# Performance work log

Hardware: AMD Instinct MI355X
Metric: run time of the kernel (lower is better)

Reference implementation:

```python
import jax, jax.numpy as jnp
import numpy as np

NUM_NOD = 6
MAX_PREV = 5
NUM_EDGE = 20  # (1+5)*5//2 + 5*(6-5)
D = 1024
H = 8
LN_EPS = 1e-6


def setup_inputs() -> dict:
    key = jax.random.key(0)
    ks = jax.random.split(key, 12)
    B, S = 8, 1024
    scale = 1.0 / np.sqrt(D)
    return {
        "inputs": jax.random.normal(ks[0], (B, S, D), jnp.float32),
        "ew": jax.random.uniform(ks[1], (NUM_NOD, 3), jnp.float32),
        "act_w": jax.random.uniform(ks[2], (NUM_NOD,), jnp.float32),
        "We": jax.random.normal(ks[3], (NUM_EDGE, D, D), jnp.float32) * scale,
        "be": jnp.zeros((NUM_EDGE, D), jnp.float32),
        "Wq": jax.random.normal(ks[4], (NUM_NOD, D, D), jnp.float32) * scale,
        "Wk": jax.random.normal(ks[5], (NUM_NOD, D, D), jnp.float32) * scale,
        "Wv": jax.random.normal(ks[6], (NUM_NOD, D, D), jnp.float32) * scale,
        "Wo": jax.random.normal(ks[7], (NUM_NOD, D, D), jnp.float32) * scale,
        "ln_g": jnp.ones((D,), jnp.float32),
        "ln_b": jnp.zeros((D,), jnp.float32),
    }


def _layernorm(x, g, b):
    mu = jnp.mean(x, axis=-1, keepdims=True)
    var = jnp.mean(jnp.square(x - mu), axis=-1, keepdims=True)
    return (x - mu) * jax.lax.rsqrt(var + LN_EPS) * g + b


def _mha(q, k, v, wq, wk, wv, wo):
    B, S, d = q.shape
    dh = d // H
    qh = (q @ wq).reshape(B, S, H, dh)
    kh = (k @ wk).reshape(B, S, H, dh)
    vh = (v @ wv).reshape(B, S, H, dh)
    scores = jnp.einsum("bqhd,bkhd->bhqk", qh, kh) / jnp.sqrt(jnp.asarray(dh, q.dtype))
    attn = jax.nn.softmax(scores, axis=-1)
    ctx = jnp.einsum("bhqk,bkhd->bqhd", attn, vh).reshape(B, S, d)
    return ctx @ wo


def reference(inputs, ew, act_w, We, be, Wq, Wk, Wv, Wo, ln_g, ln_b):
    # Fixed (deterministic) routing: node act = attention (q,k,v) for all nodes.
    # Edge op = linear (sel_ope 3). q from node c-1, k from earliest visible node,
    # v from the middle of the visible window; gated by Gumbel weights ew/act_w.
    nodes = {-1: inputs}
    lind = 0
    for c in range(NUM_NOD):
        nsrc = min(c + 1, MAX_PREV)
        snode = c - nsrc
        eq, ek, ev = lind + nsrc - 1, lind, lind + nsrc // 2
        in_q, in_k, in_v = c - 1, snode, snode + nsrc // 2
        q = ew[c, 0] * (nodes[in_q] @ We[eq] + be[eq])
        k = ew[c, 1] * (nodes[in_k] @ We[ek] + be[ek])
        v = ew[c, 2] * (nodes[in_v] @ We[ev] + be[ev])
        o = _mha(q, k, v, Wq[c], Wk[c], Wv[c], Wo[c])
        nodes[c] = act_w[c] * o + q  # gated attention + residual
        lind += nsrc
    # only node 5 is unconsumed under this routing
    out = nodes[NUM_NOD - 1]
    return _layernorm(out, ln_g, ln_b)
```

## Files before the change

kernel.cpp:

```cpp
#include <hip/hip_runtime.h>
#include <stdint.h>

#define DD 1024
#define MM 8192

typedef unsigned short u16;
typedef __attribute__((ext_vector_type(8))) short s16x8;
typedef __attribute__((ext_vector_type(4))) short s16x4;
typedef __attribute__((ext_vector_type(8))) __bf16 bf16x8;
typedef __attribute__((ext_vector_type(4))) float f32x4;

__device__ inline u16 f2bf(float f) {
  uint32_t u = __builtin_bit_cast(uint32_t, f);
  u += 0x7fffu + ((u >> 16) & 1u);
  return (u16)(u >> 16);
}
__device__ inline u16 f2bf_rn(float f) {
  return __builtin_bit_cast(u16, (__bf16)f);
}
__device__ inline float bf2f(u16 h) {
  return __builtin_bit_cast(float, (uint32_t)h << 16);
}
__device__ inline f32x4 mfma32(s16x8 a, s16x8 b, f32x4 c) {
  return __builtin_amdgcn_mfma_f32_16x16x32_bf16(
      __builtin_bit_cast(bf16x8, a), __builtin_bit_cast(bf16x8, b), c, 0, 0, 0);
}

__global__ __launch_bounds__(256) void k_cvt(const float* __restrict__ in,
                                             u16* __restrict__ out, int n8) {
  int i = blockIdx.x * 256 + threadIdx.x;
  if (i >= n8) return;
  const float4* p = (const float4*)in;
  float4 a = p[2 * i], b = p[2 * i + 1];
  union { s16x8 v; u16 u[8]; } r;
  r.u[0] = f2bf(a.x); r.u[1] = f2bf(a.y); r.u[2] = f2bf(a.z); r.u[3] = f2bf(a.w);
  r.u[4] = f2bf(b.x); r.u[5] = f2bf(b.y); r.u[6] = f2bf(b.z); r.u[7] = f2bf(b.w);
  ((s16x8*)out)[i] = r.v;
}

struct CvtSrcs { const float* p[15]; };
__global__ __launch_bounds__(256) void k_cvtN(CvtSrcs cs, u16* __restrict__ dst) {
  int z = blockIdx.y;
  const float4* p = (const float4*)cs.p[z];
  u16* out = dst + (size_t)z * DD * DD;
  int i = blockIdx.x * 256 + threadIdx.x;
  float4 a = p[2 * i], b = p[2 * i + 1];
  union { s16x8 v; u16 u[8]; } r;
  r.u[0] = f2bf(a.x); r.u[1] = f2bf(a.y); r.u[2] = f2bf(a.z); r.u[3] = f2bf(a.w);
  r.u[4] = f2bf(b.x); r.u[5] = f2bf(b.y); r.u[6] = f2bf(b.z); r.u[7] = f2bf(b.w);
  ((s16x8*)out)[i] = r.v;
}

struct WSrcs { const float* p[18]; };
__global__ __launch_bounds__(256) void k_wtransN(WSrcs ws, u16* __restrict__ pool) {
  __shared__ u16 t[32][33];
  int m = blockIdx.z;
  const float* src = ws.p[m];
  u16* dst = pool + (size_t)m * DD * DD;
  int c0 = blockIdx.x * 32, r0 = blockIdx.y * 32;
  int tx = threadIdx.x, ty = threadIdx.y;
  #pragma unroll
  for (int j = 0; j < 4; ++j)
    t[ty + j * 8][tx] = f2bf(src[(size_t)(r0 + ty + j * 8) * DD + c0 + tx]);
  __syncthreads();
  #pragma unroll
  for (int j = 0; j < 4; ++j)
    dst[(size_t)(c0 + ty + j * 8) * DD + r0 + tx] = t[tx][ty + j * 8];
}

struct BiasArgs { const float* be[18]; };
__global__ __launch_bounds__(256) void k_biasN(BiasArgs ba, const u16* __restrict__ wt,
                                               float* __restrict__ outv) {
  int z = blockIdx.y, n = blockIdx.x * 256 + threadIdx.x;
  const u16* row = wt + (size_t)z * DD * DD + (size_t)n * DD;
  const float* be = ba.be[z];
  float acc = 0.0f;
  for (int k8 = 0; k8 < DD / 8; ++k8) {
    s16x8 w = *(const s16x8*)(row + k8 * 8);
    const float4* bp = (const float4*)(be + k8 * 8);
    float4 b0 = bp[0], b1 = bp[1];
    acc += b0.x * bf2f((u16)w[0]) + b0.y * bf2f((u16)w[1]) +
           b0.z * bf2f((u16)w[2]) + b0.w * bf2f((u16)w[3]) +
           b1.x * bf2f((u16)w[4]) + b1.y * bf2f((u16)w[5]) +
           b1.z * bf2f((u16)w[6]) + b1.w * bf2f((u16)w[7]);
  }
  outv[(size_t)z * DD + n] = acc;
}

struct CombArgs { const u16* a[18]; const u16* b[18]; u16* cbase; };
__global__ __launch_bounds__(256, 2) void k_gemmC(CombArgs ca) {
  const u16* A = ca.a[blockIdx.z];
  const u16* Bt = ca.b[blockIdx.z];
  u16* C = ca.cbase + (size_t)blockIdx.z * DD * DD;
  __shared__ u16 As[128 * 64];
  __shared__ u16 Bs[128 * 64];
  const int tid = threadIdx.x;
  const int lane = tid & 63, wave = tid >> 6;
  const int g = lane >> 4, r15 = lane & 15;
  const int m0 = blockIdx.x * 128, n0 = blockIdx.y * 128;
  const int wm = (wave >> 1) * 64, wn = (wave & 1) * 64;
  f32x4 acc[4][4] = {};
  for (int kt = 0; kt < 16; ++kt) {
    const int k0 = kt * 64;
    __syncthreads();
    #pragma unroll
    for (int i = 0; i < 4; ++i) {
      int c = tid + i * 256;
      int row = c >> 3, kc = (c & 7) ^ (row & 7);
      __builtin_amdgcn_global_load_lds(
          (__attribute__((address_space(1))) void*)(A + (size_t)(m0 + row) * DD + k0 + kc * 8),
          (__attribute__((address_space(3))) void*)(As + c * 8), 16, 0, 0);
    }
    #pragma unroll
    for (int i = 0; i < 4; ++i) {
      int c = tid + i * 256;
      int row = c >> 3, kc = (c & 7) ^ (row & 7);
      __builtin_amdgcn_global_load_lds(
          (__attribute__((address_space(1))) void*)(Bt + (size_t)(n0 + row) * DD + k0 + kc * 8),
          (__attribute__((address_space(3))) void*)(Bs + c * 8), 16, 0, 0);
    }
    __syncthreads();
    #pragma unroll
    for (int ks = 0; ks < 2; ++ks) {
      s16x8 af[4], bfr[4];
      #pragma unroll
      for (int f = 0; f < 4; ++f) {
        int row = wm + f * 16 + r15;
        int kc = (ks * 4 + g) ^ (row & 7);
        af[f] = *(const s16x8*)(As + row * 64 + kc * 8);
        int rowb = wn + f * 16 + r15;
        int kcb = (ks * 4 + g) ^ (rowb & 7);
        bfr[f] = *(const s16x8*)(Bs + rowb * 64 + kcb * 8);
      }
      #pragma unroll
      for (int fm = 0; fm < 4; ++fm)
        #pragma unroll
        for (int fn = 0; fn < 4; ++fn)
          acc[fm][fn] = mfma32(af[fm], bfr[fn], acc[fm][fn]);
    }
  }
  #pragma unroll
  for (int fm = 0; fm < 4; ++fm)
    #pragma unroll
    for (int fn = 0; fn < 4; ++fn) {
      int col = n0 + wn + fn * 16 + r15;
      #pragma unroll
      for (int j = 0; j < 4; ++j) {
        int row = m0 + wm + fm * 16 + g * 4 + j;
        C[(size_t)row * DD + col] = f2bf(acc[fm][fn][j]);
      }
    }
}

struct GemmJob {
  const u16* A; const u16* Bt; const float* bias; const u16* resid;
  float* f32out;
  u16* out0; const float* s0p; float s0c;
  u16* out1; const float* s1p;
  u16* out2; const float* s2p;
  u16* vtout;
};
struct GemmBatch { GemmJob j[3]; };

__global__ __launch_bounds__(256, 2) void k_gemmN(GemmBatch gb) {
  const GemmJob jb = gb.j[blockIdx.z];
  __shared__ u16 As[128 * 64];
  __shared__ u16 Bs[128 * 64];
  const int tid = threadIdx.x;
  const int lane = tid & 63, wave = tid >> 6;
  const int g = lane >> 4, r15 = lane & 15;
  const int m0 = blockIdx.x * 128, n0 = blockIdx.y * 128;
  const int wm = (wave >> 1) * 64, wn = (wave & 1) * 64;
  f32x4 acc[4][4] = {};
  for (int kt = 0; kt < 16; ++kt) {
    const int k0 = kt * 64;
    __syncthreads();
    #pragma unroll
    for (int i = 0; i < 4; ++i) {
      int c = tid + i * 256;
      int row = c >> 3, kc = (c & 7) ^ (row & 7);
      __builtin_amdgcn_global_load_lds(
          (__attribute__((address_space(1))) void*)(jb.A + (size_t)(m0 + row) * DD + k0 + kc * 8),
          (__attribute__((address_space(3))) void*)(As + c * 8), 16, 0, 0);
    }
    #pragma unroll
    for (int i = 0; i < 4; ++i) {
      int c = tid + i * 256;
      int row = c >> 3, kc = (c & 7) ^ (row & 7);
      __builtin_amdgcn_global_load_lds(
          (__attribute__((address_space(1))) void*)(jb.Bt + (size_t)(n0 + row) * DD + k0 + kc * 8),
          (__attribute__((address_space(3))) void*)(Bs + c * 8), 16, 0, 0);
    }
    __syncthreads();
    #pragma unroll
    for (int ks = 0; ks < 2; ++ks) {
      s16x8 af[4], bfr[4];
      #pragma unroll
      for (int f = 0; f < 4; ++f) {
        int row = wm + f * 16 + r15;
        int kc = (ks * 4 + g) ^ (row & 7);
        af[f] = *(const s16x8*)(As + row * 64 + kc * 8);
        int rowb = wn + f * 16 + r15;
        int kcb = (ks * 4 + g) ^ (rowb & 7);
        bfr[f] = *(const s16x8*)(Bs + rowb * 64 + kcb * 8);
      }
      #pragma unroll
      for (int fm = 0; fm < 4; ++fm)
        #pragma unroll
        for (int fn = 0; fn < 4; ++fn)
          acc[fm][fn] = mfma32(af[fm], bfr[fn], acc[fm][fn]);
    }
  }
  const float s0 = jb.s0c * (jb.s0p ? jb.s0p[0] : 1.0f);
  if (jb.vtout) {
    #pragma unroll
    for (int fm = 0; fm < 4; ++fm) {
      #pragma unroll
      for (int fn = 0; fn < 4; ++fn) {
        int col = n0 + wn + fn * 16 + r15;
        float bcol = jb.bias ? jb.bias[col] : 0.0f;
        int row0 = m0 + wm + fm * 16 + g * 4;
        int b_ = row0 >> 10, h_ = col >> 7, d_ = col & 127, s_ = row0 & 1023;
        union { s16x4 v; u16 u[4]; } q4;
        #pragma unroll
        for (int j = 0; j < 4; ++j) q4.u[j] = f2bf(s0 * (acc[fm][fn][j] + bcol));
        *(s16x4*)(jb.vtout + (((size_t)(b_ * 8 + h_) * 128 + d_) << 10) + s_) = q4.v;
      }
    }
    return;
  }
  const float s1 = (jb.s1p ? jb.s1p[0] : 1.0f);
  const float s2 = (jb.s2p ? jb.s2p[0] : 1.0f);
  #pragma unroll
  for (int fm = 0; fm < 4; ++fm) {
    #pragma unroll
    for (int fn = 0; fn < 4; ++fn) {
      int col = n0 + wn + fn * 16 + r15;
      float bcol = jb.bias ? jb.bias[col] : 0.0f;
      #pragma unroll
      for (int j = 0; j < 4; ++j) {
        int row = m0 + wm + fm * 16 + g * 4 + j;
        size_t idx = (size_t)row * DD + col;
        float v = acc[fm][fn][j] + bcol;
        float v0 = s0 * v + (jb.resid ? bf2f(jb.resid[idx]) : 0.0f);
        if (jb.out0) jb.out0[idx] = f2bf(v0);
        if (jb.f32out) jb.f32out[idx] = v0;
        if (jb.out1) jb.out1[idx] = f2bf(s1 * v);
        if (jb.out2) jb.out2[idx] = f2bf(s2 * v);
      }
    }
  }
}

__global__ __launch_bounds__(256, 2) void k_attn(
    const u16* __restrict__ qp, const u16* __restrict__ kp,
    const u16* __restrict__ vt, u16* __restrict__ ctx) {
  __shared__ u16 Ks[2][64 * 128];
  __shared__ u16 Vs[128 * 72];
  const int lin = blockIdx.y * gridDim.x + blockIdx.x;
  const int m = lin >> 3;
  const int bh = (lin & 7) * 8 + (m & 7);
  const int q0 = (m >> 3) * 128;
  const int b = bh >> 3, h = bh & 7;
  const int tid = threadIdx.x, lane = tid & 63, wave = tid >> 6;
  const int g = lane >> 4, r15 = lane & 15;
  s16x8 qf[2][4];
  #pragma unroll
  for (int qg = 0; qg < 2; ++qg) {
    const u16* qb = qp + (size_t)(b * 1024 + q0 + wave * 32 + qg * 16 + r15) * DD + h * 128;
    #pragma unroll
    for (int kk = 0; kk < 4; ++kk) qf[qg][kk] = *(const s16x8*)(qb + kk * 32 + g * 8);
  }
  f32x4 o0[8] = {}, o1[8] = {};
  float mrow0 = -1e30f, lrow0 = 0.0f, mrow1 = -1e30f, lrow1 = 0.0f;
  const u16* kpb = kp + (size_t)b * 1024 * DD + h * 128;
  const u16* vtb = vt + (size_t)bh * 128 * 1024;

  s16x8 vreg[4];
  auto stageK = [&](int t, int buf) {
    #pragma unroll
    for (int i = 0; i < 4; ++i) {
      int c = tid + i * 256;
      int row = c >> 4, kc = (c & 15) ^ (row & 7);
      __builtin_amdgcn_global_load_lds(
          (__attribute__((address_space(1))) void*)(kpb + (size_t)(t * 64 + row) * DD + kc * 8),
          (__attribute__((address_space(3))) void*)(Ks[buf] + c * 8), 16, 0, 0);
    }
  };
  auto loadV = [&](int t) {
    #pragma unroll
    for (int i = 0; i < 4; ++i) {
      int c = tid + i * 256;
      int row = c >> 3, kc = c & 7;
      vreg[i] = *(const s16x8*)(vtb + (size_t)row * 1024 + t * 64 + kc * 8);
    }
  };
  auto writeV = [&]() {
    #pragma unroll
    for (int i = 0; i < 4; ++i) {
      int c = tid + i * 256;
      int row = c >> 3, kc = c & 7;
      *(s16x8*)(Vs + row * 72 + kc * 8) = vreg[i];
    }
  };

  stageK(0, 0);
  loadV(0);
  writeV();
  __syncthreads();

  union pk_t { s16x8 v; u16 u[8]; };
  for (int t = 0; t < 16; ++t) {
    const int cur = t & 1;
    if (t < 15) {
      stageK(t + 1, cur ^ 1);
      loadV(t + 1);
    }
    f32x4 s0[4] = {}, s1[4] = {};
    __builtin_amdgcn_s_setprio(1);
    #pragma unroll
    for (int sub = 0; sub < 4; ++sub) {
      const int krow = sub * 16 + r15;
      #pragma unroll
      for (int kk = 0; kk < 4; ++kk) {
        int slot = (kk * 4 + g) ^ (krow & 7);
        s16x8 kf = *(const s16x8*)(Ks[cur] + krow * 128 + slot * 8);
        s0[sub] = mfma32(kf, qf[0][kk], s0[sub]);
        s1[sub] = mfma32(kf, qf[1][kk], s1[sub]);
      }
    }
    __builtin_amdgcn_s_setprio(0);
    pk_t pa0[2], pa1[2];
    {
      float tm = -1e30f;
      #pragma unroll
      for (int sub = 0; sub < 4; ++sub)
        tm = fmaxf(fmaxf(fmaxf(s0[sub][0], s0[sub][1]), fmaxf(s0[sub][2], s0[sub][3])), tm);
      tm = fmaxf(tm, __shfl_xor(tm, 16));
      tm = fmaxf(tm, __shfl_xor(tm, 32));
      if (!__all(tm - mrow0 <= 8.0f)) {
        float mnew = fmaxf(mrow0, tm);
        float corr = exp2f(mrow0 - mnew);
        lrow0 *= corr;
        #pragma unroll
        for (int j = 0; j < 4; ++j) {
          float cj = __shfl(corr, (lane & 48) + g * 4 + j);
          #pragma unroll
          for (int dt = 0; dt < 8; ++dt) o0[dt][j] *= cj;
        }
        mrow0 = mnew;
      }
      float ps = 0.0f;
      #pragma unroll
      for (int sub = 0; sub < 4; ++sub)
        #pragma unroll
        for (int j = 0; j < 4; ++j) {
          float pe = exp2f(s0[sub][j] - mrow0);
          ps += pe;
          pa0[sub >> 1].u[(sub & 1) * 4 + j] = f2bf_rn(pe);
        }
      ps += __shfl_xor(ps, 16);
      ps += __shfl_xor(ps, 32);
      lrow0 += ps;
    }
    {
      float tm = -1e30f;
      #pragma unroll
      for (int sub = 0; sub < 4; ++sub)
        tm = fmaxf(fmaxf(fmaxf(s1[sub][0], s1[sub][1]), fmaxf(s1[sub][2], s1[sub][3])), tm);
      tm = fmaxf(tm, __shfl_xor(tm, 16));
      tm = fmaxf(tm, __shfl_xor(tm, 32));
      if (!__all(tm - mrow1 <= 8.0f)) {
        float mnew = fmaxf(mrow1, tm);
        float corr = exp2f(mrow1 - mnew);
        lrow1 *= corr;
        #pragma unroll
        for (int j = 0; j < 4; ++j) {
          float cj = __shfl(corr, (lane & 48) + g * 4 + j);
          #pragma unroll
          for (int dt = 0; dt < 8; ++dt) o1[dt][j] *= cj;
        }
        mrow1 = mnew;
      }
      float ps = 0.0f;
      #pragma unroll
      for (int sub = 0; sub < 4; ++sub)
        #pragma unroll
        for (int j = 0; j < 4; ++j) {
          float pe = exp2f(s1[sub][j] - mrow1);
          ps += pe;
          pa1[sub >> 1].u[(sub & 1) * 4 + j] = f2bf_rn(pe);
        }
      ps += __shfl_xor(ps, 16);
      ps += __shfl_xor(ps, 32);
      lrow1 += ps;
    }
    __builtin_amdgcn_s_setprio(1);
    #pragma unroll
    for (int p01 = 0; p01 < 2; ++p01) {
      #pragma unroll
      for (int dt = 0; dt < 8; ++dt) {
        union { s16x8 v; s16x4 h[2]; } vv;
        const u16* vbase = Vs + (dt * 16 + r15) * 72 + p01 * 32 + g * 4;
        vv.h[0] = *(const s16x4*)(vbase);
        vv.h[1] = *(const s16x4*)(vbase + 16);
        o0[dt] = mfma32(pa0[p01].v, vv.v, o0[dt]);
        o1[dt] = mfma32(pa1[p01].v, vv.v, o1[dt]);
      }
    }
    __builtin_amdgcn_s_setprio(0);
    __syncthreads();
    if (t < 15) {
      writeV();
      __syncthreads();
    }
  }
  {
    float inv = 1.0f / lrow0;
    #pragma unroll
    for (int j = 0; j < 4; ++j) {
      float cj = __shfl(inv, (lane & 48) + g * 4 + j);
      size_t row = (size_t)(b * 1024 + q0 + wave * 32 + g * 4 + j);
      #pragma unroll
      for (int dt = 0; dt < 8; ++dt)
        ctx[row * DD + h * 128 + dt * 16 + r15] = f2bf(o0[dt][j] * cj);
    }
  }
  {
    float inv = 1.0f / lrow1;
    #pragma unroll
    for (int j = 0; j < 4; ++j) {
      float cj = __shfl(inv, (lane & 48) + g * 4 + j);
      size_t row = (size_t)(b * 1024 + q0 + wave * 32 + 16 + g * 4 + j);
      #pragma unroll
      for (int dt = 0; dt < 8; ++dt)
        ctx[row * DD + h * 128 + dt * 16 + r15] = f2bf(o1[dt][j] * cj);
    }
  }
}

__global__ __launch_bounds__(256) void k_ln(const float* __restrict__ x,
                                            const float* __restrict__ gam,
                                            const float* __restrict__ bet,
                                            float* __restrict__ out) {
  __shared__ float red[8];
  const int row = blockIdx.x, tid = threadIdx.x, lane = tid & 63, wave = tid >> 6;
  const float4 v = ((const float4*)(x + (size_t)row * DD))[tid];
  float s = v.x + v.y + v.z + v.w;
  #pragma unroll
  for (int m = 1; m < 64; m <<= 1) s += __shfl_xor(s, m);
  if (lane == 0) red[wave] = s;
  __syncthreads();
  float mu = (red[0] + red[1] + red[2] + red[3]) * (1.0f / DD);
  float dx = v.x - mu, dy = v.y - mu, dz = v.z - mu, dw = v.w - mu;
  float q = dx * dx + dy * dy + dz * dz + dw * dw;
  #pragma unroll
  for (int m = 1; m < 64; m <<= 1) q += __shfl_xor(q, m);
  if (lane == 0) red[wave + 4] = q;
  __syncthreads();
  float var = (red[4] + red[5] + red[6] + red[7]) * (1.0f / DD);
  float inv = rsqrtf(var + 1e-6f);
  const float4 gv = ((const float4*)gam)[tid];
  const float4 bv = ((const float4*)bet)[tid];
  float4 r;
  r.x = dx * inv * gv.x + bv.x;
  r.y = dy * inv * gv.y + bv.y;
  r.z = dz * inv * gv.z + bv.z;
  r.w = dw * inv * gv.w + bv.w;
  ((float4*)(out + (size_t)row * DD))[tid] = r;
}

extern "C" void kernel_launch(void* const* d_in, const int* in_sizes, int n_in,
                              void* d_out, int out_size, void* d_ws, size_t ws_size,
                              hipStream_t stream) {
  const float* inputs = (const float*)d_in[0];
  const float* ew     = (const float*)d_in[1];
  const float* act_w  = (const float*)d_in[2];
  const float* We     = (const float*)d_in[3];
  const float* be     = (const float*)d_in[4];
  const float* Wq     = (const float*)d_in[5];
  const float* Wk     = (const float*)d_in[6];
  const float* Wv     = (const float*)d_in[7];
  const float* Wo     = (const float*)d_in[8];
  const float* ln_g   = (const float*)d_in[9];
  const float* ln_b   = (const float*)d_in[10];
  float* out = (float*)d_out;

  uint8_t* w = (uint8_t*)d_ws;
  size_t off = 0;
  auto alloc = [&](size_t bytes) {
    uint8_t* p = w + off;
    off += (bytes + 255) & ~(size_t)255;
    return p;
  };
  const size_t XB = (size_t)MM * DD * 2;
  const size_t WB = (size_t)DD * DD * 2;
  const size_t XBu = (size_t)MM * DD;
  const size_t WBu = (size_t)DD * DD;

  u16* Xbuf[5];
  for (int i = 0; i < 5; ++i) Xbuf[i] = (u16*)alloc(XB);
  u16* Comb  = (u16*)alloc(18 * WB);
  u16* rot   = (u16*)alloc(4 * WB);
  float* biasv = (float*)alloc(18 * DD * 4);
  u16* S     = (u16*)alloc(5 * XB);
  if (off > ws_size) {
    (void)hipMemsetAsync(d_out, 0x7F, (size_t)out_size * 4, stream);
    return;
  }
  u16* Xb[6] = {Xbuf[0], Xbuf[1], Xbuf[2], Xbuf[3], Xbuf[4], Xbuf[0]};
  u16* qb = S, * ctxb = S + XBu, * qpb = S + 2 * XBu, * kpb = S + 3 * XBu,
     * vtb = S + 4 * XBu;
  float* n5 = (float*)qpb;
  u16* stP = S;
  u16* stW = S + 18 * WBu;

  struct Node { int sq, eq, sk, ek, sv, ev; };
  static const Node route[6] = {
      {-1, 0, -1, 0, -1, 0},
      {0, 2, -1, 1, 0, 2},
      {1, 5, -1, 3, 0, 4},
      {2, 9, -1, 6, 1, 8},
      {3, 14, -1, 10, 1, 12},
      {4, 19, 0, 15, 2, 17},
  };
  const float QS = 1.4426950408889634f * 0.088388347648318433f;

  int emap[20]; for (int i = 0; i < 20; ++i) emap[i] = -1;
  int uniq[20]; int nu = 0;
  for (int c = 0; c < 6; ++c) {
    int es[3] = {route[c].eq, route[c].ek, route[c].ev};
    for (int t = 0; t < 3; ++t)
      if (emap[es[t]] < 0) { emap[es[t]] = nu; uniq[nu++] = es[t]; }
  }

  k_cvt<<<dim3(MM * DD / 8 / 256), 256, 0, stream>>>(inputs, Xb[0], MM * DD / 8);
  WSrcs w18;
  for (int c = 0; c < 6; ++c) {
    w18.p[c * 3 + 0] = Wq + (size_t)c * WBu;
    w18.p[c * 3 + 1] = Wk + (size_t)c * WBu;
    w18.p[c * 3 + 2] = Wv + (size_t)c * WBu;
  }
  k_wtransN<<<dim3(32, 32, 18), dim3(32, 8), 0, stream>>>(w18, stP);
  CvtSrcs cv;
  for (int j = 0; j < nu; ++j) cv.p[j] = We + (size_t)uniq[j] * WBu;
  k_cvtN<<<dim3(512, nu), 256, 0, stream>>>(cv, stW);
  CombArgs ca;
  BiasArgs ba;
  for (int c = 0; c < 6; ++c) {
    int es[3] = {route[c].eq, route[c].ek, route[c].ev};
    for (int t = 0; t < 3; ++t) {
      int i = c * 3 + t;
      ca.a[i] = stP + (size_t)i * WBu;
      ca.b[i] = stW + (size_t)emap[es[t]] * WBu;
      ba.be[i] = be + (size_t)es[t] * DD;
    }
  }
  ca.cbase = Comb;
  k_gemmC<<<dim3(8, 8, 18), 256, 0, stream>>>(ca);
  k_biasN<<<dim3(4, 18), 256, 0, stream>>>(ba, stP, biasv);

  GemmJob oprojPrev{};
  for (int c = 0; c < 6; ++c) {
    const Node& nd = route[c];
    u16* qeT = rot + (size_t)(c & 1) * 2 * WBu;
    u16* WoT = qeT + WBu;
    WSrcs w2{};
    w2.p[0] = We + (size_t)nd.eq * WBu;
    w2.p[1] = Wo + (size_t)c * WBu;
    k_wtransN<<<dim3(32, 32, 2), dim3(32, 8), 0, stream>>>(w2, qeT);

    GemmJob kap = {Xb[nd.sk + 1], Comb + (size_t)(c * 3 + 1) * WBu,
                   biasv + (size_t)(c * 3 + 1) * DD, nullptr, nullptr,
                   kpb, ew + 3 * c + 1, 1.0f,
                   nullptr, nullptr, nullptr, nullptr, nullptr};
    GemmJob vap = {Xb[nd.sv + 1], Comb + (size_t)(c * 3 + 2) * WBu,
                   biasv + (size_t)(c * 3 + 2) * DD, nullptr, nullptr,
                   nullptr, ew + 3 * c + 2, 1.0f,
                   nullptr, nullptr, nullptr, nullptr, vtb};
    GemmJob qed = {Xb[nd.sq + 1], qeT, be + (size_t)nd.eq * DD, nullptr, nullptr,
                   qb, ew + 3 * c + 0, 1.0f,
                   nullptr, nullptr, nullptr, nullptr, nullptr};
    GemmJob qap = {Xb[nd.sq + 1], Comb + (size_t)(c * 3 + 0) * WBu,
                   biasv + (size_t)(c * 3 + 0) * DD, nullptr, nullptr,
                   qpb, ew + 3 * c + 0, QS,
                   nullptr, nullptr, nullptr, nullptr, nullptr};

    GemmBatch A{};
    int za = 0;
    if (c >= 1) A.j[za++] = oprojPrev;
    A.j[za++] = kap;
    if (c != 1) A.j[za++] = vap;
    k_gemmN<<<dim3(64, 8, za), 256, 0, stream>>>(A);

    GemmBatch B{};
    int zb = 0;
    if (c == 1) B.j[zb++] = vap;
    B.j[zb++] = qed;
    B.j[zb++] = qap;
    k_gemmN<<<dim3(64, 8, zb), 256, 0, stream>>>(B);

    k_attn<<<dim3(8, 64), 256, 0, stream>>>(qpb, kpb, vtb, ctxb);

    oprojPrev = GemmJob{ctxb, WoT, nullptr, qb,
                        (c == 5) ? n5 : nullptr,
                        (c < 5) ? Xb[c + 1] : nullptr, act_w + c, 1.0f,
                        nullptr, nullptr, nullptr, nullptr, nullptr};
  }
  GemmBatch F{};
  F.j[0] = oprojPrev;
  k_gemmN<<<dim3(64, 8, 1), 256, 0, stream>>>(F);
  k_ln<<<dim3(MM), 256, 0, stream>>>(n5, ln_g, ln_b, out);
}
```

Baseline: 1.173 ms.

## Replace GEMM with 256x256-tile, 8-wave double-buffered pipelined kernel

Replaces the 128x128 single-buffered GEMM with a 256x256 tile kernel using 512 threads, 128KB LDS double buffering, and interleaved global->LDS prefetch of the next k-tiles between MFMA phases with setprio hints. The goal is to hide load latency behind compute and increase data reuse per LDS byte. The trade-off is fewer blocks (128 per job, against 256 CUs), so occupancy is lower and CU utilisation may suffer for single-job batches.

```diff
diff --git a/kernel.cpp b/kernel.cpp
--- a/kernel.cpp
+++ b/kernel.cpp
@@ -162,68 +162,131 @@
 };
 struct GemmBatch { GemmJob j[3]; };
 
-__global__ __launch_bounds__(256, 2) void k_gemmN(GemmBatch gb) {
+__global__ __launch_bounds__(512) void k_gemm8(GemmBatch gb) {
   const GemmJob jb = gb.j[blockIdx.z];
-  __shared__ u16 As[128 * 64];
-  __shared__ u16 Bs[128 * 64];
+  __shared__ u16 lds[65536];
   const int tid = threadIdx.x;
   const int lane = tid & 63, wave = tid >> 6;
   const int g = lane >> 4, r15 = lane & 15;
-  const int m0 = blockIdx.x * 128, n0 = blockIdx.y * 128;
-  const int wm = (wave >> 1) * 64, wn = (wave & 1) * 64;
-  f32x4 acc[4][4] = {};
-  for (int kt = 0; kt < 16; ++kt) {
-    const int k0 = kt * 64;
-    __syncthreads();
-    #pragma unroll
-    for (int i = 0; i < 4; ++i) {
-      int c = tid + i * 256;
-      int row = c >> 3, kc = (c & 7) ^ (row & 7);
+  const int wm = wave >> 2, wn = wave & 3;
+  const int m0 = blockIdx.x * 256, n0 = blockIdx.y * 256;
+  const int sXor = r15 & 7;
+
+  auto stage = [&](const u16* base, int rowbase, int t, int dst_u16) {
+    #pragma unroll
+    for (int l = 0; l < 2; ++l) {
+      int c = tid + l * 512;
+      int row = c >> 3, slot = c & 7;
+      int gch = slot ^ (row & 7);
       __builtin_amdgcn_global_load_lds(
-          (__attribute__((address_space(1))) void*)(jb.A + (size_t)(m0 + row) * DD + k0 + kc * 8),
-          (__attribute__((address_space(3))) void*)(As + c * 8), 16, 0, 0);
-    }
-    #pragma unroll
-    for (int i = 0; i < 4; ++i) {
-      int c = tid + i * 256;
-      int row = c >> 3, kc = (c & 7) ^ (row & 7);
-      __builtin_amdgcn_global_load_lds(
-          (__attribute__((address_space(1))) void*)(jb.Bt + (size_t)(n0 + row) * DD + k0 + kc * 8),
-          (__attribute__((address_space(3))) void*)(Bs + c * 8), 16, 0, 0);
-    }
-    __syncthreads();
-    #pragma unroll
-    for (int ks = 0; ks < 2; ++ks) {
-      s16x8 af[4], bfr[4];
-      #pragma unroll
-      for (int f = 0; f < 4; ++f) {
-        int row = wm + f * 16 + r15;
-        int kc = (ks * 4 + g) ^ (row & 7);
-        af[f] = *(const s16x8*)(As + row * 64 + kc * 8);
-        int rowb = wn + f * 16 + r15;
-        int kcb = (ks * 4 + g) ^ (rowb & 7);
-        bfr[f] = *(const s16x8*)(Bs + rowb * 64 + kcb * 8);
-      }
-      #pragma unroll
-      for (int fm = 0; fm < 4; ++fm)
-        #pragma unroll
-        for (int fn = 0; fn < 4; ++fn)
-          acc[fm][fn] = mfma32(af[fm], bfr[fn], acc[fm][fn]);
-    }
-  }
+          (__attribute__((address_space(1))) void*)(base + (size_t)(rowbase + row) * DD + t * 64 + gch * 8),
+          (__attribute__((address_space(3))) void*)(lds + dst_u16 + c * 8), 16, 0, 0);
+    }
+  };
+  auto stageA = [&](int t, int h) { stage(jb.A, m0 + h * 128, t, ((t & 1) * 4 + h) * 8192); };
+  auto stageB = [&](int t, int h) { stage(jb.Bt, n0 + h * 128, t, ((t & 1) * 4 + 2 + h) * 8192); };
+
+  f32x4 acc[8][4] = {};
+  stageA(0, 0); stageA(0, 1); stageB(0, 0); stageB(0, 1);
+  stageA(1, 0); stageA(1, 1); stageB(1, 0); stageB(1, 1);
+  asm volatile("s_waitcnt vmcnt(8)" ::: "memory");
+  __builtin_amdgcn_s_barrier();
+
+  const int abase = wm * 8192;
+  const int brow = wn * 64;
+  const int bbase = 16384 + (brow >> 7) * 8192;
+  const int bhrow = brow & 127;
+
+  for (int t = 0; t < 16; ++t) {
+    const int bufo = (t & 1) * 32768;
+    s16x8 af[4][2], bf[2][2], bf2[2][2];
+    #pragma unroll
+    for (int f = 0; f < 4; ++f)
+      #pragma unroll
+      for (int ks = 0; ks < 2; ++ks)
+        af[f][ks] = *(const s16x8*)(lds + bufo + abase + (f * 16 + r15) * 64 + (((ks * 4 + g) ^ sXor) * 8));
+    #pragma unroll
+    for (int nf = 0; nf < 2; ++nf)
+      #pragma unroll
+      for (int ks = 0; ks < 2; ++ks)
+        bf[nf][ks] = *(const s16x8*)(lds + bufo + bbase + (bhrow + nf * 16 + r15) * 64 + (((ks * 4 + g) ^ sXor) * 8));
+    if (t >= 1 && t <= 14) stageA(t + 1, 0);
+    __builtin_amdgcn_s_barrier();
+    __builtin_amdgcn_s_setprio(1);
+    #pragma unroll
+    for (int f = 0; f < 4; ++f)
+      #pragma unroll
+      for (int nf = 0; nf < 2; ++nf)
+        #pragma unroll
+        for (int ks = 0; ks < 2; ++ks)
+          acc[f][nf] = mfma32(af[f][ks], bf[nf][ks], acc[f][nf]);
+    __builtin_amdgcn_s_setprio(0);
+    __builtin_amdgcn_s_barrier();
+    #pragma unroll
+    for (int nf = 0; nf < 2; ++nf)
+      #pragma unroll
+      for (int ks = 0; ks < 2; ++ks)
+        bf2[nf][ks] = *(const s16x8*)(lds + bufo + bbase + (bhrow + 32 + nf * 16 + r15) * 64 + (((ks * 4 + g) ^ sXor) * 8));
+    if (t >= 1 && t <= 14) stageA(t + 1, 1);
+    __builtin_amdgcn_s_barrier();
+    __builtin_amdgcn_s_setprio(1);
+    #pragma unroll
+    for (int f = 0; f < 4; ++f)
+      #pragma unroll
+      for (int nf = 0; nf < 2; ++nf)
+        #pragma unroll
+        for (int ks = 0; ks < 2; ++ks)
+          acc[f][nf + 2] = mfma32(af[f][ks], bf2[nf][ks], acc[f][nf + 2]);
+    __builtin_amdgcn_s_setprio(0);
+    __builtin_amdgcn_s_barrier();
+    #pragma unroll
+    for (int f = 0; f < 4; ++f)
+      #pragma unroll
+      for (int ks = 0; ks < 2; ++ks)
+        af[f][ks] = *(const s16x8*)(lds + bufo + abase + ((f + 4) * 16 + r15) * 64 + (((ks * 4 + g) ^ sXor) * 8));
+    if (t <= 13) stageB(t + 2, 0);
+    __builtin_amdgcn_s_barrier();
+    __builtin_amdgcn_s_setprio(1);
+    #pragma unroll
+    for (int f = 0; f < 4; ++f)
+      #pragma unroll
+      for (int nf = 0; nf < 2; ++nf)
+        #pragma unroll
+        for (int ks = 0; ks < 2; ++ks)
+          acc[f + 4][nf] = mfma32(af[f][ks], bf[nf][ks], acc[f + 4][nf]);
+    __builtin_amdgcn_s_setprio(0);
+    __builtin_amdgcn_s_barrier();
+    if (t <= 13) stageB(t + 2, 1);
+    __builtin_amdgcn_s_barrier();
+    __builtin_amdgcn_s_setprio(1);
+    #pragma unroll
+    for (int f = 0; f < 4; ++f)
+      #pragma unroll
+      for (int nf = 0; nf < 2; ++nf)
+        #pragma unroll
+        for (int ks = 0; ks < 2; ++ks)
+          acc[f + 4][nf + 2] = mfma32(af[f][ks], bf2[nf][ks], acc[f + 4][nf + 2]);
+    __builtin_amdgcn_s_setprio(0);
+    if (t < 15) {
+      if (t <= 13) asm volatile("s_waitcnt vmcnt(4)" ::: "memory");
+      else         asm volatile("s_waitcnt vmcnt(0)" ::: "memory");
+    }
+    __builtin_amdgcn_s_barrier();
+  }
+
   const float s0 = jb.s0c * (jb.s0p ? jb.s0p[0] : 1.0f);
   if (jb.vtout) {
     #pragma unroll
-    for (int fm = 0; fm < 4; ++fm) {
-      #pragma unroll
-      for (int fn = 0; fn < 4; ++fn) {
-        int col = n0 + wn + fn * 16 + r15;
+    for (int f = 0; f < 8; ++f) {
+      #pragma unroll
+      for (int nf = 0; nf < 4; ++nf) {
+        int col = n0 + wn * 64 + nf * 16 + r15;
         float bcol = jb.bias ? jb.bias[col] : 0.0f;
-        int row0 = m0 + wm + fm * 16 + g * 4;
+        int row0 = m0 + wm * 128 + f * 16 + g * 4;
         int b_ = row0 >> 10, h_ = col >> 7, d_ = col & 127, s_ = row0 & 1023;
         union { s16x4 v; u16 u[4]; } q4;
         #pragma unroll
-        for (int j = 0; j < 4; ++j) q4.u[j] = f2bf(s0 * (acc[fm][fn][j] + bcol));
+        for (int j = 0; j < 4; ++j) q4.u[j] = f2bf(s0 * (acc[f][nf][j] + bcol));
         *(s16x4*)(jb.vtout + (((size_t)(b_ * 8 + h_) * 128 + d_) << 10) + s_) = q4.v;
       }
     }
@@ -232,16 +295,16 @@
   const float s1 = (jb.s1p ? jb.s1p[0] : 1.0f);
   const float s2 = (jb.s2p ? jb.s2p[0] : 1.0f);
   #pragma unroll
-  for (int fm = 0; fm < 4; ++fm) {
-    #pragma unroll
-    for (int fn = 0; fn < 4; ++fn) {
-      int col = n0 + wn + fn * 16 + r15;
+  for (int f = 0; f < 8; ++f) {
+    #pragma unroll
+    for (int nf = 0; nf < 4; ++nf) {
+      int col = n0 + wn * 64 + nf * 16 + r15;
       float bcol = jb.bias ? jb.bias[col] : 0.0f;
       #pragma unroll
       for (int j = 0; j < 4; ++j) {
-        int row = m0 + wm + fm * 16 + g * 4 + j;
+        int row = m0 + wm * 128 + f * 16 + g * 4 + j;
         size_t idx = (size_t)row * DD + col;
-        float v = acc[fm][fn][j] + bcol;
+        float v = acc[f][nf][j] + bcol;
         float v0 = s0 * v + (jb.resid ? bf2f(jb.resid[idx]) : 0.0f);
         if (jb.out0) jb.out0[idx] = f2bf(v0);
         if (jb.f32out) jb.f32out[idx] = v0;
@@ -591,14 +654,14 @@
     if (c >= 1) A.j[za++] = oprojPrev;
     A.j[za++] = kap;
     if (c != 1) A.j[za++] = vap;
-    k_gemmN<<<dim3(64, 8, za), 256, 0, stream>>>(A);
+    k_gemm8<<<dim3(32, 4, za), 512, 0, stream>>>(A);
 
     GemmBatch B{};
     int zb = 0;
     if (c == 1) B.j[zb++] = vap;
     B.j[zb++] = qed;
     B.j[zb++] = qap;
-    k_gemmN<<<dim3(64, 8, zb), 256, 0, stream>>>(B);
+    k_gemm8<<<dim3(32, 4, zb), 512, 0, stream>>>(B);
 
     k_attn<<<dim3(8, 64), 256, 0, stream>>>(qpb, kpb, vtb, ctxb);
 
@@ -609,6 +672,6 @@
   }
   GemmBatch F{};
   F.j[0] = oprojPrev;
-  k_gemmN<<<dim3(64, 8, 1), 256, 0, stream>>>(F);
+  k_gemm8<<<dim3(32, 4, 1), 512, 0, stream>>>(F);
   k_ln<<<dim3(MM), 256, 0, stream>>>(n5, ln_g, ln_b, out);
 }
```

Result: slower. 1.241 ms (+5.9%).
